# Optimization experiments

Hardware: AMD Instinct MI355X
Metric: run time of the kernel (lower is better)

Reference implementation:

```python
import jax, jax.numpy as jnp
import numpy as np

C = 256
G = 32  # GroupNorm groups
EPS = 1e-6


def setup_inputs() -> dict:
    key = jax.random.key(0)
    ks = jax.random.split(key, 10)
    b, c, d, h, w = 2, C, 16, 16, 16
    s = 1.0 / np.sqrt(c)
    return {
        "x": jax.random.normal(ks[0], (b, c, d, h, w), jnp.float32),
        "gn_gamma": jnp.ones((c,), jnp.float32),
        "gn_beta": jnp.zeros((c,), jnp.float32),
        "wq": jax.random.normal(ks[1], (c, c), jnp.float32) * s,
        "bq": jax.random.normal(ks[2], (c,), jnp.float32) * 0.01,
        "wk": jax.random.normal(ks[3], (c, c), jnp.float32) * s,
        "bk": jax.random.normal(ks[4], (c,), jnp.float32) * 0.01,
        "wv": jax.random.normal(ks[5], (c, c), jnp.float32) * s,
        "bv": jax.random.normal(ks[6], (c,), jnp.float32) * 0.01,
        "wp": jax.random.normal(ks[7], (c, c), jnp.float32) * s,
        "bp": jax.random.normal(ks[8], (c,), jnp.float32) * 0.01,
    }


def _group_norm(x, gamma, beta):
    b, c, d, h, w = x.shape
    xg = x.reshape(b, G, c // G, d, h, w)
    mu = jnp.mean(xg, axis=(2, 3, 4, 5), keepdims=True)
    var = jnp.var(xg, axis=(2, 3, 4, 5), keepdims=True)
    xn = ((xg - mu) * jax.lax.rsqrt(var + EPS)).reshape(b, c, d, h, w)
    return xn * gamma[None, :, None, None, None] + beta[None, :, None, None, None]


def reference(x, gn_gamma, gn_beta, wq, bq, wk, bk, wv, bv, wp, bp):
    b, c, d, h, w = x.shape
    n = d * h * w
    hn = _group_norm(x, gn_gamma, gn_beta).reshape(b, c, n)  # (b, c, n)
    # 1x1 conv3d == channel-mixing matmul
    q = jnp.einsum("oc,bcn->bon", wq, hn) + bq[None, :, None]
    k = jnp.einsum("oc,bcn->bon", wk, hn) + bk[None, :, None]
    v = jnp.einsum("oc,bcn->bon", wv, hn) + bv[None, :, None]
    scale = c ** (-0.5)
    attn = jax.nn.softmax(jnp.einsum("bcn,bcm->bnm", q, k) * scale, axis=2)  # (b, n, m)
    # torch: h_ = bmm(v, attn^T) -> h_[b,c,n] = sum_m v[b,c,m] * attn[b,n,m]
    hv = jnp.einsum("bcm,bnm->bcn", v, attn)
    out = jnp.einsum("oc,bcn->bon", wp, hv) + bp[None, :, None]
    w_returned = jnp.transpose(attn, (0, 2, 1))  # matches torch's returned permuted w_
    return (x + out.reshape(b, c, d, h, w), w_returned)
```

## Files before the change

### kernel.cpp

```cpp
#include <hip/hip_runtime.h>


typedef __bf16 bf16_t;
typedef __bf16 bf16x8 __attribute__((ext_vector_type(8)));
typedef float floatx4 __attribute__((ext_vector_type(4)));

typedef __attribute__((address_space(1))) const unsigned int gas_u32;
typedef __attribute__((address_space(3))) unsigned int las_u32;

__device__ __forceinline__ void gl_lds16(const void* g, void* l) {
  __builtin_amdgcn_global_load_lds((gas_u32*)g, (las_u32*)l, 16, 0, 0);
}

__device__ __forceinline__ unsigned short f2bf(float f) {
  union { float f; unsigned int u; } v; v.f = f;
  return (unsigned short)((v.u + 0x7FFFu + ((v.u >> 16) & 1u)) >> 16);
}
__device__ __forceinline__ float bf2f(unsigned short u) {
  union { unsigned int u; float f; } v; v.u = ((unsigned int)u) << 16;
  return v.f;
}

__global__ void prep_kernel(const float* __restrict__ wq, const float* __restrict__ wk,
                            const float* __restrict__ wv, const float* __restrict__ wp,
                            const float* __restrict__ bq, const float* __restrict__ bk,
                            const float* __restrict__ bv, const float* __restrict__ bp,
                            const float* __restrict__ x, unsigned short* __restrict__ Astack,
                            unsigned short* __restrict__ wpbf, unsigned short* __restrict__ wvT,
                            float* __restrict__ bqkv2, float* __restrict__ bias2,
                            float* __restrict__ mean, float* __restrict__ rstd) {
  __shared__ float T[64 * 67];
  __shared__ float red[256];
  const int blk = blockIdx.x;
  const int tid = threadIdx.x;
  if (blk < 768) {
    int w = blk >> 8;
    const float* src = (w == 0) ? wq : (w == 1) ? wk : wp;
    unsigned short* dst = (w == 0) ? Astack : (w == 1) ? (Astack + 65536) : wpbf;
    int i = (blk & 255) * 256 + tid;
    dst[i] = f2bf(src[i]);
  } else if (blk < 784) {
    int t = blk - 768, tr = t >> 2, tc = t & 3;
#pragma unroll
    for (int rr = 0; rr < 16; ++rr) {
      int r = rr * 4 + (tid >> 6), c = tid & 63;
      T[r * 67 + c] = wv[(size_t)(tr * 64 + r) * 256 + tc * 64 + c];
    }
    __syncthreads();
#pragma unroll
    for (int rr = 0; rr < 16; ++rr) {
      int cc = rr * 4 + (tid >> 6), r = tid & 63;
      wvT[(size_t)(tc * 64 + cc) * 256 + tr * 64 + r] = f2bf(T[r * 67 + cc]);
    }
  } else if (blk < 848) {
    int bg = blk - 784;
    const float* p = x + (size_t)bg * 32768;
    float s = 0.f, ss = 0.f;
    for (int i = tid * 4; i < 32768; i += 1024) {
      float4 v = *(const float4*)&p[i];
      s += v.x + v.y + v.z + v.w;
      ss += v.x * v.x + v.y * v.y + v.z * v.z + v.w * v.w;
    }
    for (int off = 32; off > 0; off >>= 1) {
      s += __shfl_down(s, off);
      ss += __shfl_down(ss, off);
    }
    int wid = tid >> 6;
    if ((tid & 63) == 0) { red[wid] = s; red[64 + wid] = ss; }
    __syncthreads();
    if (tid == 0) {
      float S = red[0] + red[1] + red[2] + red[3];
      float SS = red[64] + red[65] + red[66] + red[67];
      float mu = S * (1.f / 32768.f);
      float var = SS * (1.f / 32768.f) - mu * mu;
      mean[bg] = mu;
      rstd[bg] = rsqrtf(var + 1e-6f);
    }
  } else if (blk == 848) {
    bqkv2[tid] = bq[tid];
    bqkv2[256 + tid] = bk[tid];
    bqkv2[512 + tid] = 0.f;
  } else {
    int bb = blk - 849;
    int o = bb * 64 + (tid >> 2), part = tid & 3;
    float s = 0.f;
#pragma unroll
    for (int j = 0; j < 16; ++j) {
      float4 w4 = *(const float4*)&wp[(size_t)o * 256 + part * 64 + j * 4];
      float4 b4 = *(const float4*)&bv[part * 64 + j * 4];
      s += w4.x * b4.x + w4.y * b4.y + w4.z * b4.z + w4.w * b4.w;
    }
    red[tid] = s;
    __syncthreads();
    if (part == 0) bias2[o] = bp[o] + red[tid] + red[tid + 1] + red[tid + 2] + red[tid + 3];
  }
}

__global__ void gn_apply_t_kernel(const float* __restrict__ x, const float* __restrict__ gamma,
                                  const float* __restrict__ beta, const float* __restrict__ mean,
                                  const float* __restrict__ rstd, unsigned short* __restrict__ hnT) {
  int n0 = blockIdx.x * 64, c0 = blockIdx.y * 64, b = blockIdx.z;
  int tid = threadIdx.x;
  __shared__ __align__(16) unsigned short T[64 * 72];
#pragma unroll
  for (int r = 0; r < 4; ++r) {
    int cl = (tid >> 4) + r * 16;
    int nl = (tid & 15) * 4;
    int c = c0 + cl;
    int bg = b * 32 + (c >> 3);
    float mu = mean[bg], rsd = rstd[bg], ga = gamma[c], be = beta[c];
    float4 v = *(const float4*)&x[(size_t)b * 1048576 + (size_t)c * 4096 + n0 + nl];
    ushort4 u;
    u.x = f2bf((v.x - mu) * rsd * ga + be);
    u.y = f2bf((v.y - mu) * rsd * ga + be);
    u.z = f2bf((v.z - mu) * rsd * ga + be);
    u.w = f2bf((v.w - mu) * rsd * ga + be);
    *(ushort4*)&T[cl * 72 + nl] = u;
  }
  __syncthreads();
#pragma unroll
  for (int w = 0; w < 2; ++w) {
    int nl = (tid >> 3) + w * 32;
    int cch = (tid & 7) * 8;
    unsigned short u8[8];
#pragma unroll
    for (int i = 0; i < 8; ++i) u8[i] = T[(cch + i) * 72 + nl];
    size_t o = (size_t)b * 1048576 + (size_t)(n0 + nl) * 256 + c0 + cch;
    *(ushort4*)&hnT[o] = make_ushort4(u8[0], u8[1], u8[2], u8[3]);
    *(ushort4*)&hnT[o + 4] = make_ushort4(u8[4], u8[5], u8[6], u8[7]);
  }
}

template <int BM, int BN>
__launch_bounds__(256)
__global__ void gemm_tn(const bf16_t* __restrict__ A, const bf16_t* __restrict__ B, int ldb,
                        unsigned short* __restrict__ C, int N, int K) {
  constexpr int BK = 32, LD = BK + 8;
  constexpr int WM = BM / 2, WN = BN / 2, MI = WM / 16, NI = WN / 16;
  __shared__ __align__(16) bf16_t As[BM * LD];
  __shared__ __align__(16) bf16_t Bs[BN * LD];
  const int tid = threadIdx.x;
  const int lane = tid & 63, wid = tid >> 6;
  const int quad = lane >> 4, l16 = lane & 15;
  const int m0 = blockIdx.y * BM, n0 = blockIdx.x * BN;
  const int wm0 = (wid >> 1) * WM, wn0 = (wid & 1) * WN;

  floatx4 acc[MI][NI];
#pragma unroll
  for (int i = 0; i < MI; ++i)
#pragma unroll
    for (int j = 0; j < NI; ++j) acc[i][j] = (floatx4){0.f, 0.f, 0.f, 0.f};

  const int arow = tid >> 2, akj = (tid & 3) << 3;
  for (int kt = 0; kt < K; kt += BK) {
#pragma unroll
    for (int p = 0; p < BM / 64; ++p) {
      int r = p * 64 + arow;
      *(uint4*)&As[r * LD + akj] = *(const uint4*)&A[(size_t)(m0 + r) * K + kt + akj];
    }
#pragma unroll
    for (int p = 0; p < BN / 64; ++p) {
      int r = p * 64 + arow;
      *(uint4*)&Bs[r * LD + akj] = *(const uint4*)&B[(size_t)(n0 + r) * ldb + kt + akj];
    }
    __syncthreads();
    bf16x8 af[MI], bfr[NI];
#pragma unroll
    for (int i = 0; i < MI; ++i) af[i] = *(const bf16x8*)&As[(wm0 + i * 16 + l16) * LD + quad * 8];
#pragma unroll
    for (int j = 0; j < NI; ++j) bfr[j] = *(const bf16x8*)&Bs[(wn0 + j * 16 + l16) * LD + quad * 8];
#pragma unroll
    for (int i = 0; i < MI; ++i)
#pragma unroll
      for (int j = 0; j < NI; ++j)
        acc[i][j] = __builtin_amdgcn_mfma_f32_16x16x32_bf16(af[i], bfr[j], acc[i][j], 0, 0, 0);
    __syncthreads();
  }

#pragma unroll
  for (int i = 0; i < MI; ++i) {
    int gmb = m0 + wm0 + i * 16 + quad * 4;
#pragma unroll
    for (int j = 0; j < NI; ++j) {
      int gn = n0 + wn0 + j * 16 + l16;
#pragma unroll
      for (int r = 0; r < 4; ++r) C[(size_t)(gmb + r) * N + gn] = f2bf(acc[i][j][r]);
    }
  }
}

__launch_bounds__(256)
__global__ void gemm_qkvw(const bf16_t* __restrict__ Astack, const bf16_t* __restrict__ hnT,
                          const float* __restrict__ bqkv2, unsigned short* __restrict__ qkT,
                          unsigned short* __restrict__ W2) {
  constexpr int BM = 64, BN = 128, BK = 64, MI = 2, NI = 4;
  __shared__ __align__(16) bf16_t As[BM * BK];
  __shared__ __align__(16) bf16_t Bs[BN * BK];
  const int tid = threadIdx.x;
  const int lane = tid & 63, wid = tid >> 6;
  const int quad = lane >> 4, l16 = lane & 15;
  const int b = blockIdx.z;
  const bf16_t* B = hnT + (size_t)b * 1048576;
  const int m0 = blockIdx.y * BM, n0 = blockIdx.x * BN;
  const int wm0 = (wid >> 1) * 32, wn0 = (wid & 1) * 64;
  const int srow = lane >> 3;
  const int scol = ((lane & 7) ^ srow) << 3;

  floatx4 acc[MI][NI];
#pragma unroll
  for (int i = 0; i < MI; ++i)
#pragma unroll
    for (int j = 0; j < NI; ++j) acc[i][j] = (floatx4){0.f, 0.f, 0.f, 0.f};

  for (int kt = 0; kt < 256; kt += BK) {
#pragma unroll
    for (int p = 0; p < 2; ++p) {
      int rb = wid * 16 + p * 8;
      gl_lds16(&Astack[(size_t)(m0 + rb + srow) * 256 + kt + scol], &As[rb * BK]);
    }
#pragma unroll
    for (int p = 0; p < 4; ++p) {
      int rb = wid * 32 + p * 8;
      gl_lds16(&B[(size_t)(n0 + rb + srow) * 256 + kt + scol], &Bs[rb * BK]);
    }
    __syncthreads();
#pragma unroll
    for (int ks = 0; ks < 2; ++ks) {
      bf16x8 af[MI], bfr[NI];
#pragma unroll
      for (int i = 0; i < MI; ++i) {
        int r = wm0 + i * 16 + l16;
        af[i] = *(const bf16x8*)&As[r * BK + ((((ks << 2) + quad) ^ (r & 7)) << 3)];
      }
#pragma unroll
      for (int j = 0; j < NI; ++j) {
        int r = wn0 + j * 16 + l16;
        bfr[j] = *(const bf16x8*)&Bs[r * BK + ((((ks << 2) + quad) ^ (r & 7)) << 3)];
      }
#pragma unroll
      for (int i = 0; i < MI; ++i)
#pragma unroll
        for (int j = 0; j < NI; ++j)
          acc[i][j] = __builtin_amdgcn_mfma_f32_16x16x32_bf16(af[i], bfr[j], acc[i][j], 0, 0, 0);
    }
    __syncthreads();
  }

#pragma unroll
  for (int i = 0; i < MI; ++i) {
    int gmb = m0 + wm0 + i * 16 + quad * 4;
#pragma unroll
    for (int j = 0; j < NI; ++j) {
      int gn = n0 + wn0 + j * 16 + l16;
      float v[4];
#pragma unroll
      for (int r = 0; r < 4; ++r) v[r] = acc[i][j][r] + bqkv2[gmb + r];
      if (m0 < 512) {
        ushort4 u = make_ushort4(f2bf(v[0]), f2bf(v[1]), f2bf(v[2]), f2bf(v[3]));
        *(ushort4*)&qkT[(size_t)b * 2097152 + (size_t)gn * 512 + gmb] = u;
      } else {
#pragma unroll
        for (int r = 0; r < 4; ++r)
          W2[(size_t)b * 1048576 + (size_t)(gmb - 512 + r) * 4096 + gn] = f2bf(v[r]);
      }
    }
  }
}

__launch_bounds__(256)
__global__ void gemm_qk_exp(const bf16_t* __restrict__ qkT, unsigned short* __restrict__ EbfT,
                            float* __restrict__ psum) {
  constexpr int BM = 128, BN = 128, BK = 64, MI = 4, NI = 4;
  constexpr int LDC = BM + 8;
  __shared__ __align__(16) char SMEM[BM * LDC * 2];
  bf16_t* As = (bf16_t*)SMEM;
  bf16_t* Bs = (bf16_t*)SMEM + BM * BK;
  unsigned short* Ct = (unsigned short*)SMEM;
  const int tid = threadIdx.x;
  const int lane = tid & 63, wid = tid >> 6;
  const int quad = lane >> 4, l16 = lane & 15;
  const int b = blockIdx.z;
  const bf16_t* A = qkT + (size_t)b * 2097152 + 256;
  const bf16_t* B = qkT + (size_t)b * 2097152;
  const int m0 = blockIdx.y * BM, n0 = blockIdx.x * BN;
  const int wm0 = (wid >> 1) * 64, wn0 = (wid & 1) * 64;
  const int srow = lane >> 3;
  const int scol = ((lane & 7) ^ srow) << 3;

  floatx4 acc[MI][NI];
#pragma unroll
  for (int i = 0; i < MI; ++i)
#pragma unroll
    for (int j = 0; j < NI; ++j) acc[i][j] = (floatx4){0.f, 0.f, 0.f, 0.f};

  for (int kt = 0; kt < 256; kt += BK) {
#pragma unroll
    for (int p = 0; p < 4; ++p) {
      int rb = wid * 32 + p * 8;
      gl_lds16(&A[(size_t)(m0 + rb + srow) * 512 + kt + scol], &As[rb * BK]);
      gl_lds16(&B[(size_t)(n0 + rb + srow) * 512 + kt + scol], &Bs[rb * BK]);
    }
    __syncthreads();
#pragma unroll
    for (int ks = 0; ks < 2; ++ks) {
      bf16x8 af[MI], bfr[NI];
#pragma unroll
      for (int i = 0; i < MI; ++i) {
        int r = wm0 + i * 16 + l16;
        af[i] = *(const bf16x8*)&As[r * BK + ((((ks << 2) + quad) ^ (r & 7)) << 3)];
      }
#pragma unroll
      for (int j = 0; j < NI; ++j) {
        int r = wn0 + j * 16 + l16;
        bfr[j] = *(const bf16x8*)&Bs[r * BK + ((((ks << 2) + quad) ^ (r & 7)) << 3)];
      }
#pragma unroll
      for (int i = 0; i < MI; ++i)
#pragma unroll
        for (int j = 0; j < NI; ++j)
          acc[i][j] = __builtin_amdgcn_mfma_f32_16x16x32_bf16(af[i], bfr[j], acc[i][j], 0, 0, 0);
    }
    __syncthreads();
  }

  float csum[NI] = {0.f, 0.f, 0.f, 0.f};
#pragma unroll
  for (int i = 0; i < MI; ++i) {
    int ml = wm0 + i * 16 + quad * 4;
#pragma unroll
    for (int j = 0; j < NI; ++j) {
      int nl = wn0 + j * 16 + l16;
      float e[4];
#pragma unroll
      for (int r = 0; r < 4; ++r) e[r] = __expf(acc[i][j][r] * 0.0625f);
      csum[j] += (e[0] + e[1]) + (e[2] + e[3]);
      *(ushort4*)&Ct[nl * LDC + ml] = make_ushort4(f2bf(e[0]), f2bf(e[1]), f2bf(e[2]), f2bf(e[3]));
    }
  }
#pragma unroll
  for (int j = 0; j < NI; ++j) {
    csum[j] += __shfl_xor(csum[j], 16);
    csum[j] += __shfl_xor(csum[j], 32);
  }
  if (quad == 0) {
    int my = blockIdx.y * 2 + (wid >> 1);
#pragma unroll
    for (int j = 0; j < NI; ++j)
      psum[((size_t)b * 64 + my) * 4096 + n0 + wn0 + j * 16 + l16] = csum[j];
  }
  __syncthreads();
#pragma unroll
  for (int pass = 0; pass < 8; ++pass) {
    int row = pass * 16 + (tid >> 4);
    int mc = (tid & 15) * 8;
    uint4 v = *(uint4*)&Ct[row * LDC + mc];
    *(uint4*)&EbfT[(size_t)b * 16777216 + (size_t)(n0 + row) * 4096 + m0 + mc] = v;
  }
}

__launch_bounds__(256)
__global__ void gemm_pv_fused(const bf16_t* __restrict__ W2, const bf16_t* __restrict__ EbfT,
                              const float* __restrict__ psum, const float* __restrict__ bias2,
                              const float* __restrict__ x, float* __restrict__ out0,
                              float* __restrict__ attn) {
  constexpr int BK = 128;
  __shared__ __align__(16) bf16_t As[128 * BK];
  __shared__ __align__(16) bf16_t Bs[32 * BK];
  __shared__ float rs[32];
  __shared__ float sred[256];
  const int tid = threadIdx.x;
  const int lane = tid & 63, wid = tid >> 6;
  const int quad = lane >> 4, l16 = lane & 15;
  const int b = blockIdx.z, mb = blockIdx.y;
  const int n0 = blockIdx.x * 32;
  const size_t eb = (size_t)b * 16777216;

  {
    int nl = tid & 31, rp = tid >> 5;
    float s = 0.f;
#pragma unroll
    for (int i = 0; i < 8; ++i) s += psum[((size_t)b * 64 + rp * 8 + i) * 4096 + n0 + nl];
    sred[tid] = s;
  }
  __syncthreads();
  if (tid < 32) {
    float s = 0.f;
#pragma unroll
    for (int i = 0; i < 8; ++i) s += sred[i * 32 + tid];
    rs[tid] = 1.f / s;
  }
  __syncthreads();

  const int wm0 = (wid >> 1) * 64, wn0 = (wid & 1) * 16;
  const int r4 = lane >> 4, s16 = lane & 15;
  const bf16_t* Wb = W2 + (size_t)b * 1048576 + (size_t)(mb * 128) * 4096;
  const bf16_t* Eb = EbfT + eb;
  const int pml = mb * 64 + (tid >> 2);
  const int pn4 = (tid & 3) * 8;

  floatx4 acc[4];
#pragma unroll
  for (int i = 0; i < 4; ++i) acc[i] = (floatx4){0.f, 0.f, 0.f, 0.f};

  for (int kt = 0; kt < 4096; kt += BK) {
#pragma unroll
    for (int p = 0; p < 8; ++p) {
      int rb = wid * 32 + p * 4;
      int key = ((p & 1) << 2) | r4;
      gl_lds16(&Wb[(size_t)(rb + r4) * 4096 + kt + ((s16 ^ key) << 3)], &As[rb * BK]);
    }
#pragma unroll
    for (int p = 0; p < 2; ++p) {
      int rb = wid * 8 + p * 4;
      int key = ((p & 1) << 2) | r4;
      gl_lds16(&Eb[(size_t)(n0 + rb + r4) * 4096 + kt + ((s16 ^ key) << 3)], &Bs[rb * BK]);
    }
    __syncthreads();
    {
      const unsigned short* Bu = (const unsigned short*)Bs;
      float o[8];
#pragma unroll
      for (int j = 0; j < 8; ++j) {
        int n = pn4 + j;
        o[j] = bf2f(Bu[n * BK + ((((pml >> 3) ^ (n & 7)) << 3) | (pml & 7))]) * rs[n];
      }
      size_t ro = eb + (size_t)(kt + pml) * 4096 + n0 + pn4;
      *(float4*)&attn[ro] = make_float4(o[0], o[1], o[2], o[3]);
      *(float4*)&attn[ro + 4] = make_float4(o[4], o[5], o[6], o[7]);
    }
#pragma unroll
    for (int ks = 0; ks < 4; ++ks) {
      int rn = wn0 + l16;
      bf16x8 bfr = *(const bf16x8*)&Bs[rn * BK + ((((ks << 2) + quad) ^ (rn & 7)) << 3)];
#pragma unroll
      for (int i = 0; i < 4; ++i) {
        int rm = wm0 + i * 16 + l16;
        bf16x8 af = *(const bf16x8*)&As[rm * BK + ((((ks << 2) + quad) ^ (rm & 7)) << 3)];
        acc[i] = __builtin_amdgcn_mfma_f32_16x16x32_bf16(af, bfr, acc[i], 0, 0, 0);
      }
    }
    __syncthreads();
  }

  const float* xb = x + (size_t)b * 1048576;
  float* ob = out0 + (size_t)b * 1048576;
  int gn = n0 + wn0 + l16;
  float cs = rs[wn0 + l16];
#pragma unroll
  for (int i = 0; i < 4; ++i) {
    int o = mb * 128 + wm0 + i * 16 + quad * 4;
#pragma unroll
    for (int r = 0; r < 4; ++r)
      ob[(size_t)(o + r) * 4096 + gn] =
          acc[i][r] * cs + bias2[o + r] + xb[(size_t)(o + r) * 4096 + gn];
  }
}

extern "C" void kernel_launch(void* const* d_in, const int* in_sizes, int n_in,
                              void* d_out, int out_size, void* d_ws, size_t ws_size,
                              hipStream_t stream) {
  const float* x = (const float*)d_in[0];
  const float* gamma = (const float*)d_in[1];
  const float* beta = (const float*)d_in[2];
  const float* wq = (const float*)d_in[3];
  const float* bq = (const float*)d_in[4];
  const float* wk = (const float*)d_in[5];
  const float* bk = (const float*)d_in[6];
  const float* wv = (const float*)d_in[7];
  const float* bv = (const float*)d_in[8];
  const float* wp = (const float*)d_in[9];
  const float* bp = (const float*)d_in[10];

  float* out0 = (float*)d_out;
  float* attn = (float*)d_out + 2097152;

  char* ws = (char*)d_ws;
  unsigned short* Astack = (unsigned short*)(ws + 0);
  unsigned short* wpbf = (unsigned short*)(ws + 393216);
  unsigned short* wvT = (unsigned short*)(ws + 524288);
  float* bqkv2 = (float*)(ws + 655360);
  float* bias2 = (float*)(ws + 658432);
  float* gmean = (float*)(ws + 659456);
  float* grstd = (float*)(ws + 659712);
  float* psum = (float*)(ws + 1048576);
  unsigned short* hnT = (unsigned short*)(ws + 4194304);
  unsigned short* qkT = (unsigned short*)(ws + 8388608);
  unsigned short* W2 = (unsigned short*)(ws + 16777216);
  unsigned short* EbfT = (unsigned short*)(ws + 20971520);

  prep_kernel<<<853, 256, 0, stream>>>(wq, wk, wv, wp, bq, bk, bv, bp, x, Astack, wpbf, wvT,
                                       bqkv2, bias2, gmean, grstd);

  gemm_tn<64, 128><<<dim3(2, 4, 1), 256, 0, stream>>>((const bf16_t*)wpbf, (const bf16_t*)wvT, 256,
                                                      Astack + 131072, 256, 256);

  gn_apply_t_kernel<<<dim3(64, 4, 2), 256, 0, stream>>>(x, gamma, beta, gmean, grstd, hnT);

  gemm_qkvw<<<dim3(32, 12, 2), 256, 0, stream>>>((const bf16_t*)Astack, (const bf16_t*)hnT, bqkv2,
                                                 qkT, W2);

  gemm_qk_exp<<<dim3(32, 32, 2), 256, 0, stream>>>((const bf16_t*)qkT, EbfT, psum);

  gemm_pv_fused<<<dim3(128, 2, 2), 256, 0, stream>>>((const bf16_t*)W2, (const bf16_t*)EbfT, psum,
                                                     bias2, x, out0, attn);
}
```

Before: 263.0 us.

## Double-buffer PV GEMM loads, remap blocks, fold Wp·Wv product into prep kernel

The fused PV/attention-output kernel now streams W2 and E tiles through a two-stage LDS ring with BK=64. It uses explicit vmcnt waits and raw barriers so the next tile's global-to-LDS loads overlap the current tile's MFMAs and attention writes. The grid is flattened to 1D with a remapping of batch, m-block and n-block, likely to improve cache locality across concurrently running blocks. Separately, the Wp·Wv weight product is now computed in fp32 directly inside the prep kernel, which removes the wvT transpose, the wpbf conversion and a separate small GEMM launch. That fp32 loop is a scalar, serial 256-term dot product per thread.

```diff
diff --git a/kernel.cpp b/kernel.cpp
--- a/kernel.cpp
+++ b/kernel.cpp
@@ -26,34 +26,19 @@
                             const float* __restrict__ bq, const float* __restrict__ bk,
                             const float* __restrict__ bv, const float* __restrict__ bp,
                             const float* __restrict__ x, unsigned short* __restrict__ Astack,
-                            unsigned short* __restrict__ wpbf, unsigned short* __restrict__ wvT,
                             float* __restrict__ bqkv2, float* __restrict__ bias2,
                             float* __restrict__ mean, float* __restrict__ rstd) {
-  __shared__ float T[64 * 67];
   __shared__ float red[256];
   const int blk = blockIdx.x;
   const int tid = threadIdx.x;
-  if (blk < 768) {
+  if (blk < 512) {
     int w = blk >> 8;
-    const float* src = (w == 0) ? wq : (w == 1) ? wk : wp;
-    unsigned short* dst = (w == 0) ? Astack : (w == 1) ? (Astack + 65536) : wpbf;
+    const float* src = (w == 0) ? wq : wk;
+    unsigned short* dst = Astack + w * 65536;
     int i = (blk & 255) * 256 + tid;
     dst[i] = f2bf(src[i]);
-  } else if (blk < 784) {
-    int t = blk - 768, tr = t >> 2, tc = t & 3;
-#pragma unroll
-    for (int rr = 0; rr < 16; ++rr) {
-      int r = rr * 4 + (tid >> 6), c = tid & 63;
-      T[r * 67 + c] = wv[(size_t)(tr * 64 + r) * 256 + tc * 64 + c];
-    }
-    __syncthreads();
-#pragma unroll
-    for (int rr = 0; rr < 16; ++rr) {
-      int cc = rr * 4 + (tid >> 6), r = tid & 63;
-      wvT[(size_t)(tc * 64 + cc) * 256 + tr * 64 + r] = f2bf(T[r * 67 + cc]);
-    }
-  } else if (blk < 848) {
-    int bg = blk - 784;
+  } else if (blk < 576) {
+    int bg = blk - 512;
     const float* p = x + (size_t)bg * 32768;
     float s = 0.f, ss = 0.f;
     for (int i = tid * 4; i < 32768; i += 1024) {
@@ -76,12 +61,12 @@
       mean[bg] = mu;
       rstd[bg] = rsqrtf(var + 1e-6f);
     }
-  } else if (blk == 848) {
+  } else if (blk == 576) {
     bqkv2[tid] = bq[tid];
     bqkv2[256 + tid] = bk[tid];
     bqkv2[512 + tid] = 0.f;
-  } else {
-    int bb = blk - 849;
+  } else if (blk < 581) {
+    int bb = blk - 577;
     int o = bb * 64 + (tid >> 2), part = tid & 3;
     float s = 0.f;
 #pragma unroll
@@ -93,6 +78,13 @@
     red[tid] = s;
     __syncthreads();
     if (part == 0) bias2[o] = bp[o] + red[tid] + red[tid + 1] + red[tid + 2] + red[tid + 3];
+  } else {
+    int o = blk - 581;
+    const float* wpo = wp + (size_t)o * 256;
+    float acc = 0.f;
+#pragma unroll 4
+    for (int k = 0; k < 256; ++k) acc = fmaf(wpo[k], wv[(size_t)k * 256 + tid], acc);
+    Astack[(size_t)(512 + o) * 256 + tid] = f2bf(acc);
   }
 }
 
@@ -128,64 +120,6 @@
     size_t o = (size_t)b * 1048576 + (size_t)(n0 + nl) * 256 + c0 + cch;
     *(ushort4*)&hnT[o] = make_ushort4(u8[0], u8[1], u8[2], u8[3]);
     *(ushort4*)&hnT[o + 4] = make_ushort4(u8[4], u8[5], u8[6], u8[7]);
-  }
-}
-
-template <int BM, int BN>
-__launch_bounds__(256)
-__global__ void gemm_tn(const bf16_t* __restrict__ A, const bf16_t* __restrict__ B, int ldb,
-                        unsigned short* __restrict__ C, int N, int K) {
-  constexpr int BK = 32, LD = BK + 8;
-  constexpr int WM = BM / 2, WN = BN / 2, MI = WM / 16, NI = WN / 16;
-  __shared__ __align__(16) bf16_t As[BM * LD];
-  __shared__ __align__(16) bf16_t Bs[BN * LD];
-  const int tid = threadIdx.x;
-  const int lane = tid & 63, wid = tid >> 6;
-  const int quad = lane >> 4, l16 = lane & 15;
-  const int m0 = blockIdx.y * BM, n0 = blockIdx.x * BN;
-  const int wm0 = (wid >> 1) * WM, wn0 = (wid & 1) * WN;
-
-  floatx4 acc[MI][NI];
-#pragma unroll
-  for (int i = 0; i < MI; ++i)
-#pragma unroll
-    for (int j = 0; j < NI; ++j) acc[i][j] = (floatx4){0.f, 0.f, 0.f, 0.f};
-
-  const int arow = tid >> 2, akj = (tid & 3) << 3;
-  for (int kt = 0; kt < K; kt += BK) {
-#pragma unroll
-    for (int p = 0; p < BM / 64; ++p) {
-      int r = p * 64 + arow;
-      *(uint4*)&As[r * LD + akj] = *(const uint4*)&A[(size_t)(m0 + r) * K + kt + akj];
-    }
-#pragma unroll
-    for (int p = 0; p < BN / 64; ++p) {
-      int r = p * 64 + arow;
-      *(uint4*)&Bs[r * LD + akj] = *(const uint4*)&B[(size_t)(n0 + r) * ldb + kt + akj];
-    }
-    __syncthreads();
-    bf16x8 af[MI], bfr[NI];
-#pragma unroll
-    for (int i = 0; i < MI; ++i) af[i] = *(const bf16x8*)&As[(wm0 + i * 16 + l16) * LD + quad * 8];
-#pragma unroll
-    for (int j = 0; j < NI; ++j) bfr[j] = *(const bf16x8*)&Bs[(wn0 + j * 16 + l16) * LD + quad * 8];
-#pragma unroll
-    for (int i = 0; i < MI; ++i)
-#pragma unroll
-      for (int j = 0; j < NI; ++j)
-        acc[i][j] = __builtin_amdgcn_mfma_f32_16x16x32_bf16(af[i], bfr[j], acc[i][j], 0, 0, 0);
-    __syncthreads();
-  }
-
-#pragma unroll
-  for (int i = 0; i < MI; ++i) {
-    int gmb = m0 + wm0 + i * 16 + quad * 4;
-#pragma unroll
-    for (int j = 0; j < NI; ++j) {
-      int gn = n0 + wn0 + j * 16 + l16;
-#pragma unroll
-      for (int r = 0; r < 4; ++r) C[(size_t)(gmb + r) * N + gn] = f2bf(acc[i][j][r]);
-    }
   }
 }
 
@@ -363,16 +297,19 @@
                               const float* __restrict__ psum, const float* __restrict__ bias2,
                               const float* __restrict__ x, float* __restrict__ out0,
                               float* __restrict__ attn) {
-  constexpr int BK = 128;
-  __shared__ __align__(16) bf16_t As[128 * BK];
-  __shared__ __align__(16) bf16_t Bs[32 * BK];
+  constexpr int BK = 64;
+  __shared__ __align__(16) bf16_t As[2][128 * BK];
+  __shared__ __align__(16) bf16_t Bs[2][32 * BK];
   __shared__ float rs[32];
   __shared__ float sred[256];
   const int tid = threadIdx.x;
   const int lane = tid & 63, wid = tid >> 6;
   const int quad = lane >> 4, l16 = lane & 15;
-  const int b = blockIdx.z, mb = blockIdx.y;
-  const int n0 = blockIdx.x * 32;
+  const int d = blockIdx.x;
+  const int xk = d & 7, idx = d >> 3;
+  const int b = xk >> 2;
+  const int mb = idx >> 5;
+  const int n0 = (((xk & 3) << 5) | (idx & 31)) * 32;
   const size_t eb = (size_t)b * 16777216;
 
   {
@@ -392,55 +329,74 @@
   __syncthreads();
 
   const int wm0 = (wid >> 1) * 64, wn0 = (wid & 1) * 16;
-  const int r4 = lane >> 4, s16 = lane & 15;
+  const int srow = lane >> 3;
+  const int scol = ((lane & 7) ^ srow) << 3;
   const bf16_t* Wb = W2 + (size_t)b * 1048576 + (size_t)(mb * 128) * 4096;
   const bf16_t* Eb = EbfT + eb;
-  const int pml = mb * 64 + (tid >> 2);
-  const int pn4 = (tid & 3) * 8;
+  const int pml = mb * 32 + (tid >> 3);
+  const int pnc = (tid & 7) * 4;
+  float rsv[4];
+#pragma unroll
+  for (int j = 0; j < 4; ++j) rsv[j] = rs[pnc + j];
 
   floatx4 acc[4];
 #pragma unroll
   for (int i = 0; i < 4; ++i) acc[i] = (floatx4){0.f, 0.f, 0.f, 0.f};
 
-  for (int kt = 0; kt < 4096; kt += BK) {
-#pragma unroll
-    for (int p = 0; p < 8; ++p) {
-      int rb = wid * 32 + p * 4;
-      int key = ((p & 1) << 2) | r4;
-      gl_lds16(&Wb[(size_t)(rb + r4) * 4096 + kt + ((s16 ^ key) << 3)], &As[rb * BK]);
-    }
-#pragma unroll
-    for (int p = 0; p < 2; ++p) {
-      int rb = wid * 8 + p * 4;
-      int key = ((p & 1) << 2) | r4;
-      gl_lds16(&Eb[(size_t)(n0 + rb + r4) * 4096 + kt + ((s16 ^ key) << 3)], &Bs[rb * BK]);
-    }
-    __syncthreads();
+#define PV_STAGE(c, kt)                                                              \
+  {                                                                                  \
+    _Pragma("unroll") for (int p = 0; p < 4; ++p) {                                  \
+      int rb = wid * 32 + p * 8;                                                     \
+      gl_lds16(&Wb[(size_t)(rb + srow) * 4096 + (kt) + scol], &As[c][rb * BK]);      \
+    }                                                                                \
+    {                                                                                \
+      int rb = wid * 8;                                                              \
+      gl_lds16(&Eb[(size_t)(n0 + rb + srow) * 4096 + (kt) + scol], &Bs[c][rb * BK]); \
+    }                                                                                \
+  }
+
+  PV_STAGE(0, 0);
+  for (int t = 0; t < 64; ++t) {
+    const int c = t & 1;
+    const int kt = t * BK;
+    if (t < 63) PV_STAGE(c ^ 1, kt + BK);
+    if (t == 0) {
+      asm volatile("s_waitcnt vmcnt(5)" ::: "memory");
+    } else if (t < 63) {
+      asm volatile("s_waitcnt vmcnt(6)" ::: "memory");
+    } else {
+      asm volatile("s_waitcnt vmcnt(1)" ::: "memory");
+    }
+    __builtin_amdgcn_sched_barrier(0);
+    __builtin_amdgcn_s_barrier();
     {
-      const unsigned short* Bu = (const unsigned short*)Bs;
-      float o[8];
-#pragma unroll
-      for (int j = 0; j < 8; ++j) {
-        int n = pn4 + j;
-        o[j] = bf2f(Bu[n * BK + ((((pml >> 3) ^ (n & 7)) << 3) | (pml & 7))]) * rs[n];
-      }
-      size_t ro = eb + (size_t)(kt + pml) * 4096 + n0 + pn4;
-      *(float4*)&attn[ro] = make_float4(o[0], o[1], o[2], o[3]);
-      *(float4*)&attn[ro + 4] = make_float4(o[4], o[5], o[6], o[7]);
-    }
-#pragma unroll
-    for (int ks = 0; ks < 4; ++ks) {
+      const unsigned short* Bu = (const unsigned short*)Bs[c];
+      float o[4];
+#pragma unroll
+      for (int j = 0; j < 4; ++j) {
+        int n = pnc + j;
+        o[j] = bf2f(Bu[n * BK + ((((pml >> 3) ^ (n & 7)) << 3) | (pml & 7))]) * rsv[j];
+      }
+      *(float4*)&attn[eb + (size_t)(kt + pml) * 4096 + n0 + pnc] =
+          make_float4(o[0], o[1], o[2], o[3]);
+    }
+    {
       int rn = wn0 + l16;
-      bf16x8 bfr = *(const bf16x8*)&Bs[rn * BK + ((((ks << 2) + quad) ^ (rn & 7)) << 3)];
-#pragma unroll
-      for (int i = 0; i < 4; ++i) {
-        int rm = wm0 + i * 16 + l16;
-        bf16x8 af = *(const bf16x8*)&As[rm * BK + ((((ks << 2) + quad) ^ (rm & 7)) << 3)];
-        acc[i] = __builtin_amdgcn_mfma_f32_16x16x32_bf16(af, bfr, acc[i], 0, 0, 0);
-      }
-    }
-    __syncthreads();
-  }
+#pragma unroll
+      for (int ks = 0; ks < 2; ++ks) {
+        bf16x8 bfr = *(const bf16x8*)&Bs[c][rn * BK + ((((ks << 2) + quad) ^ (rn & 7)) << 3)];
+#pragma unroll
+        for (int i = 0; i < 4; ++i) {
+          int rm = wm0 + i * 16 + l16;
+          bf16x8 af = *(const bf16x8*)&As[c][rm * BK + ((((ks << 2) + quad) ^ (rm & 7)) << 3)];
+          acc[i] = __builtin_amdgcn_mfma_f32_16x16x32_bf16(af, bfr, acc[i], 0, 0, 0);
+        }
+      }
+    }
+    __builtin_amdgcn_sched_barrier(0);
+    __builtin_amdgcn_s_barrier();
+  }
+#undef PV_STAGE
 
   const float* xb = x + (size_t)b * 1048576;
   float* ob = out0 + (size_t)b * 1048576;
@@ -476,8 +432,6 @@
 
   char* ws = (char*)d_ws;
   unsigned short* Astack = (unsigned short*)(ws + 0);
-  unsigned short* wpbf = (unsigned short*)(ws + 393216);
-  unsigned short* wvT = (unsigned short*)(ws + 524288);
   float* bqkv2 = (float*)(ws + 655360);
   float* bias2 = (float*)(ws + 658432);
   float* gmean = (float*)(ws + 659456);
@@ -488,11 +442,8 @@
   unsigned short* W2 = (unsigned short*)(ws + 16777216);
   unsigned short* EbfT = (unsigned short*)(ws + 20971520);
 
-  prep_kernel<<<853, 256, 0, stream>>>(wq, wk, wv, wp, bq, bk, bv, bp, x, Astack, wpbf, wvT,
+  prep_kernel<<<837, 256, 0, stream>>>(wq, wk, wv, wp, bq, bk, bv, bp, x, Astack,
                                        bqkv2, bias2, gmean, grstd);
-
-  gemm_tn<64, 128><<<dim3(2, 4, 1), 256, 0, stream>>>((const bf16_t*)wpbf, (const bf16_t*)wvT, 256,
-                                                      Astack + 131072, 256, 256);
 
   gn_apply_t_kernel<<<dim3(64, 4, 2), 256, 0, stream>>>(x, gamma, beta, gmean, grstd, hnT);
 
@@ -501,6 +452,6 @@
 
   gemm_qk_exp<<<dim3(32, 32, 2), 256, 0, stream>>>((const bf16_t*)qkT, EbfT, psum);
 
-  gemm_pv_fused<<<dim3(128, 2, 2), 256, 0, stream>>>((const bf16_t*)W2, (const bf16_t*)EbfT, psum,
-                                                     bias2, x, out0, attn);
-}
+  gemm_pv_fused<<<512, 256, 0, stream>>>((const bf16_t*)W2, (const bf16_t*)EbfT, psum,
+                                         bias2, x, out0, attn);
+}
```

Result: slower. 268.6 us (+2.1%).
